# Performance work log

Hardware: AMD Instinct MI355X
Metric: run time of the kernel (lower is better)

The kernel has to match this reference:

```python
import jax, jax.numpy as jnp
import numpy as np

B, S, IN, OUT = 4, 4096, 4096, 4096

def setup_inputs() -> dict:
    key = jax.random.key(0)
    k1, k2, k3 = jax.random.split(key, 3)
    x = jax.random.normal(k1, (B, S, IN), dtype=jnp.float32)
    # packed ternary weight: (sign+1) in {0,1,2}, stored as small int
    packed_w = jax.random.randint(k2, (OUT, IN), 0, 3, dtype=jnp.int32)
    # alpha = mean(|W|) surrogate; act_scale = max|x|/127 surrogate
    alpha = jnp.float32(0.02)
    act_scale = jnp.float32(4.0 / 127.0)
    bias = jax.random.normal(k3, (OUT,), dtype=jnp.float32)
    return {"x": x, "packed_w": packed_w, "alpha": alpha, "act_scale": act_scale, "bias": bias}

def reference(x, packed_w, alpha, act_scale, bias):
    # Activation fake-quant (int8 symmetric): round(x/scale), clamp, dequant.
    # torch uses act_scale.item() -> scale is a constant w.r.t. autodiff.
    scale = jax.lax.stop_gradient(jnp.maximum(act_scale, 1e-5))
    x_int = jnp.clip(jnp.round(x / scale), -127.0, 127.0)
    x_dq = jnp.nan_to_num(x_int * scale, nan=0.0, posinf=10000.0, neginf=-10000.0)
    # Ternary weight dequant: (packed - 1) * alpha, values in {-a, 0, +a}
    w = (packed_w.astype(jnp.float32) - 1.0) * alpha  # [OUT, IN]
    # F.linear: x @ W^T + b
    return jnp.einsum('bsi,oi->bso', x_dq, w) + bias
```

## Files before the change

### kernel.cpp

```cpp
#include <hip/hip_runtime.h>
#include <hip/hip_bf16.h>

typedef int v4i __attribute__((ext_vector_type(4)));

#define M_DIM 16384
#define N_DIM 4096
#define K_DIM 4096
#define BM 256
#define BN 256
#define BKB 128
#define NT (K_DIM / BKB)

__global__ void quant_x_kernel(const float4* __restrict__ x, int* __restrict__ q,
                               const float* __restrict__ act_scale, int n4) {
  const float s = fmaxf(act_scale[0], 1e-5f);
  int i = blockIdx.x * blockDim.x + threadIdx.x;
  const int stride = gridDim.x * blockDim.x;
  for (; i < n4; i += stride) {
    float4 v = x[i];
    int b0 = (int)fminf(fmaxf(rintf(v.x / s), -127.f), 127.f);
    int b1 = (int)fminf(fmaxf(rintf(v.y / s), -127.f), 127.f);
    int b2 = (int)fminf(fmaxf(rintf(v.z / s), -127.f), 127.f);
    int b3 = (int)fminf(fmaxf(rintf(v.w / s), -127.f), 127.f);
    q[i] = (b0 & 0xff) | ((b1 & 0xff) << 8) | ((b2 & 0xff) << 16) | ((b3 & 0xff) << 24);
  }
}

__global__ void pack_w_kernel(const int4* __restrict__ w, int* __restrict__ q, int n4) {
  int i = blockIdx.x * blockDim.x + threadIdx.x;
  const int stride = gridDim.x * blockDim.x;
  for (; i < n4; i += stride) {
    int4 v = w[i];
    q[i] = ((v.x - 1) & 0xff) | (((v.y - 1) & 0xff) << 8) |
           (((v.z - 1) & 0xff) << 16) | (((v.w - 1) & 0xff) << 24);
  }
}

__global__ __launch_bounds__(512, 2) void bitlinear_gemm(
    const signed char* __restrict__ A,
    const signed char* __restrict__ B,
    const float* __restrict__ bias,
    const float* __restrict__ alpha_p,
    const float* __restrict__ act_scale_p,
    float* __restrict__ out) {
  __shared__ __align__(16) signed char As[2][BM * BKB];
  __shared__ __align__(16) signed char Bs[2][BN * BKB];

  const int t = threadIdx.x;
  const int lane = t & 63, wid = t >> 6;
  const int wm = wid >> 2, wn = wid & 3;
  const int l15 = lane & 15, l4 = lane >> 4;

  const int nwg = (M_DIM / BM) * (N_DIM / BN);
  const int wg = (blockIdx.x & 7) * (nwg >> 3) + (blockIdx.x >> 3);
  const int bm = wg / (N_DIM / BN);
  const int bn = wg % (N_DIM / BN);

  const signed char* aGl = A + ((size_t)(bm * BM + (t >> 3))) * K_DIM + (t & 7) * 16;
  const signed char* bGl = B + ((size_t)(bn * BN + (t >> 3))) * K_DIM + (t & 7) * 16;
  const int wrOff = (t >> 3) * 128 + (((t & 7) ^ ((t >> 3) & 7)) * 16);

  v4i sA[4], sB[4];

#define GL_A(u, P) sA[u] = *(const v4i*)((P) + (size_t)((u) * 64) * K_DIM)
#define GL_B(u, P) sB[u] = *(const v4i*)((P) + (size_t)((u) * 64) * K_DIM)
#define WR_A(BUF) { _Pragma("unroll") for (int u = 0; u < 4; ++u) \
    *(v4i*)&As[BUF][u * 8192 + wrOff] = sA[u]; }
#define WR_B(BUF) { _Pragma("unroll") for (int u = 0; u < 4; ++u) \
    *(v4i*)&Bs[BUF][u * 8192 + wrOff] = sB[u]; }

  const int l7 = l15 & 7;
  const int soK0 = ((0 + l4) ^ l7) * 16;
  const int soK1 = ((4 + l4) ^ l7) * 16;
  const int aRd = (wm * 128 + l15) * BKB;
  const int bRd = (wn * 64 + l15) * BKB;

  v4i acc[8][4] = {};
  v4i bF[4][2], aF[2][2];

#define LOAD_B(buf) \
  { _Pragma("unroll") for (int nc = 0; nc < 4; ++nc) { \
      bF[nc][0] = *(const v4i*)&Bs[buf][bRd + nc * 2048 + soK0]; \
      bF[nc][1] = *(const v4i*)&Bs[buf][bRd + nc * 2048 + soK1]; } }

#define LOAD_A(buf, q) \
  aF[0][0] = *(const v4i*)&As[buf][aRd + (2*(q)) * 2048 + soK0]; \
  aF[0][1] = *(const v4i*)&As[buf][aRd + (2*(q)) * 2048 + soK1]; \
  aF[1][0] = *(const v4i*)&As[buf][aRd + (2*(q)+1) * 2048 + soK0]; \
  aF[1][1] = *(const v4i*)&As[buf][aRd + (2*(q)+1) * 2048 + soK1];

#define MFMA_Q(q) \
  { _Pragma("unroll") for (int nc = 0; nc < 4; ++nc) { \
      acc[2*(q)][nc]   = __builtin_amdgcn_mfma_i32_16x16x64_i8(aF[0][0], bF[nc][0], acc[2*(q)][nc], 0, 0, 0); \
      acc[2*(q)][nc]   = __builtin_amdgcn_mfma_i32_16x16x64_i8(aF[0][1], bF[nc][1], acc[2*(q)][nc], 0, 0, 0); \
      acc[2*(q)+1][nc] = __builtin_amdgcn_mfma_i32_16x16x64_i8(aF[1][0], bF[nc][0], acc[2*(q)+1][nc], 0, 0, 0); \
      acc[2*(q)+1][nc] = __builtin_amdgcn_mfma_i32_16x16x64_i8(aF[1][1], bF[nc][1], acc[2*(q)+1][nc], 0, 0, 0); } }

#define BAR __builtin_amdgcn_s_barrier()

#define TILE_BODY(BUF, PA, PB) do { \
    LOAD_B(BUF); LOAD_A(BUF, 0); \
    GL_B(0, PB); GL_B(1, PB); \
    __builtin_amdgcn_s_setprio(1); MFMA_Q(0); __builtin_amdgcn_s_setprio(0); \
    LOAD_A(BUF, 1); \
    GL_B(2, PB); GL_B(3, PB); \
    __builtin_amdgcn_s_setprio(1); MFMA_Q(1); __builtin_amdgcn_s_setprio(0); \
    LOAD_A(BUF, 2); \
    GL_A(0, PA); GL_A(1, PA); GL_A(2, PA); GL_A(3, PA); \
    __builtin_amdgcn_s_setprio(1); MFMA_Q(2); __builtin_amdgcn_s_setprio(0); \
    WR_B(BUF^1); \
    LOAD_A(BUF, 3); \
    __builtin_amdgcn_s_setprio(1); MFMA_Q(3); __builtin_amdgcn_s_setprio(0); \
    WR_A(BUF^1); \
    asm volatile("s_waitcnt lgkmcnt(0)" ::: "memory"); \
    BAR; \
  } while (0)

  GL_B(0, bGl); GL_B(1, bGl); GL_B(2, bGl); GL_B(3, bGl);
  GL_A(0, aGl); GL_A(1, aGl); GL_A(2, aGl); GL_A(3, aGl);
  asm volatile("s_waitcnt vmcnt(0)" ::: "memory");
  WR_B(0); WR_A(0);
  asm volatile("s_waitcnt lgkmcnt(0)" ::: "memory");
  BAR;
  __builtin_amdgcn_sched_barrier(0);

  const signed char* aGk = aGl;
  const signed char* bGk = bGl;
  for (int it = 0; it < NT / 2 - 1; ++it) {
    TILE_BODY(0, aGk + BKB,     bGk + BKB);
    TILE_BODY(1, aGk + 2 * BKB, bGk + 2 * BKB);
    aGk += 2 * BKB; bGk += 2 * BKB;
  }
  TILE_BODY(0, aGk + BKB, bGk + BKB);
  TILE_BODY(1, aGk + BKB, bGk + BKB);

  const float sA_ = fmaxf(act_scale_p[0], 1e-5f) * alpha_p[0];
  const int gn0 = bn * BN + wn * 64 + l15;
  const int gm0 = bm * BM + wm * 128 + l4 * 4;
#pragma unroll
  for (int nc = 0; nc < 4; ++nc) {
    const float bv = bias[gn0 + nc * 16];
#pragma unroll
    for (int mr = 0; mr < 8; ++mr) {
#pragma unroll
      for (int r = 0; r < 4; ++r) {
        const int gm = gm0 + mr * 16 + r;
        out[(size_t)gm * N_DIM + gn0 + nc * 16] = (float)acc[mr][nc][r] * sA_ + bv;
      }
    }
  }
}

extern "C" void kernel_launch(void* const* d_in, const int* in_sizes, int n_in,
                              void* d_out, int out_size, void* d_ws, size_t ws_size,
                              hipStream_t stream) {
  const float* x      = (const float*)d_in[0];
  const int*   pw     = (const int*)d_in[1];
  const float* alpha  = (const float*)d_in[2];
  const float* act_sc = (const float*)d_in[3];
  const float* bias   = (const float*)d_in[4];
  float* out = (float*)d_out;

  signed char* x8 = (signed char*)d_ws;
  signed char* w8 = (signed char*)d_ws + (size_t)M_DIM * K_DIM;

  quant_x_kernel<<<2048, 256, 0, stream>>>((const float4*)x, (int*)x8, act_sc, M_DIM * K_DIM / 4);
  pack_w_kernel<<<2048, 256, 0, stream>>>((const int4*)pw, (int*)w8, N_DIM * K_DIM / 4);

  dim3 grid((M_DIM / BM) * (N_DIM / BN));
  bitlinear_gemm<<<grid, 512, 0, stream>>>(x8, w8, bias, alpha, act_sc, out);
}
```

Before: 380.1 us.

## Load A fragments directly from global memory into registers, bypassing LDS

The int8 activation tile no longer goes through shared memory. Each wave loads its MFMA A-operand fragments straight from global memory into two ping-ponged register sets, prefetching the next quarter during the current MFMA group. This removes the LDS writes and reads for A and halves the LDS footprint, which may allow higher occupancy. In exchange, A data that was shared through LDS is now re-read from global or L2 by each of the four waves in a row, and the fragment loads are uncoalesced 16-byte strided accesses whose latency must hide behind a single MFMA quarter.

```diff
diff --git a/kernel.cpp b/kernel.cpp
--- a/kernel.cpp
+++ b/kernel.cpp
@@ -43,7 +43,6 @@
     const float* __restrict__ alpha_p,
     const float* __restrict__ act_scale_p,
     float* __restrict__ out) {
-  __shared__ __align__(16) signed char As[2][BM * BKB];
   __shared__ __align__(16) signed char Bs[2][BN * BKB];
 
   const int t = threadIdx.x;
@@ -56,83 +55,78 @@
   const int bm = wg / (N_DIM / BN);
   const int bn = wg % (N_DIM / BN);
 
-  const signed char* aGl = A + ((size_t)(bm * BM + (t >> 3))) * K_DIM + (t & 7) * 16;
   const signed char* bGl = B + ((size_t)(bn * BN + (t >> 3))) * K_DIM + (t & 7) * 16;
   const int wrOff = (t >> 3) * 128 + (((t & 7) ^ ((t >> 3) & 7)) * 16);
+  v4i sB[4];
 
-  v4i sA[4], sB[4];
-
-#define GL_A(u, P) sA[u] = *(const v4i*)((P) + (size_t)((u) * 64) * K_DIM)
 #define GL_B(u, P) sB[u] = *(const v4i*)((P) + (size_t)((u) * 64) * K_DIM)
-#define WR_A(BUF) { _Pragma("unroll") for (int u = 0; u < 4; ++u) \
-    *(v4i*)&As[BUF][u * 8192 + wrOff] = sA[u]; }
 #define WR_B(BUF) { _Pragma("unroll") for (int u = 0; u < 4; ++u) \
     *(v4i*)&Bs[BUF][u * 8192 + wrOff] = sB[u]; }
 
   const int l7 = l15 & 7;
   const int soK0 = ((0 + l4) ^ l7) * 16;
   const int soK1 = ((4 + l4) ^ l7) * 16;
-  const int aRd = (wm * 128 + l15) * BKB;
   const int bRd = (wn * 64 + l15) * BKB;
 
+  const signed char* aBase = A + ((size_t)(bm * BM + wm * 128 + l15)) * K_DIM + l4 * 16;
+
+  v4i aP[4], aQ[4];
+#define AL(R, mi2, KOFF) \
+  R[0] = *(const v4i*)(aBase + (size_t)(mi2) * 16 * K_DIM + (KOFF)); \
+  R[1] = *(const v4i*)(aBase + (size_t)(mi2) * 16 * K_DIM + (KOFF) + 64); \
+  R[2] = *(const v4i*)(aBase + (size_t)((mi2) + 1) * 16 * K_DIM + (KOFF)); \
+  R[3] = *(const v4i*)(aBase + (size_t)((mi2) + 1) * 16 * K_DIM + (KOFF) + 64);
+
   v4i acc[8][4] = {};
-  v4i bF[4][2], aF[2][2];
+  v4i bF[4][2];
 
 #define LOAD_B(buf) \
   { _Pragma("unroll") for (int nc = 0; nc < 4; ++nc) { \
       bF[nc][0] = *(const v4i*)&Bs[buf][bRd + nc * 2048 + soK0]; \
       bF[nc][1] = *(const v4i*)&Bs[buf][bRd + nc * 2048 + soK1]; } }
 
-#define LOAD_A(buf, q) \
-  aF[0][0] = *(const v4i*)&As[buf][aRd + (2*(q)) * 2048 + soK0]; \
-  aF[0][1] = *(const v4i*)&As[buf][aRd + (2*(q)) * 2048 + soK1]; \
-  aF[1][0] = *(const v4i*)&As[buf][aRd + (2*(q)+1) * 2048 + soK0]; \
-  aF[1][1] = *(const v4i*)&As[buf][aRd + (2*(q)+1) * 2048 + soK1];
-
-#define MFMA_Q(q) \
+#define MFMA_Q(q, R) \
   { _Pragma("unroll") for (int nc = 0; nc < 4; ++nc) { \
-      acc[2*(q)][nc]   = __builtin_amdgcn_mfma_i32_16x16x64_i8(aF[0][0], bF[nc][0], acc[2*(q)][nc], 0, 0, 0); \
-      acc[2*(q)][nc]   = __builtin_amdgcn_mfma_i32_16x16x64_i8(aF[0][1], bF[nc][1], acc[2*(q)][nc], 0, 0, 0); \
-      acc[2*(q)+1][nc] = __builtin_amdgcn_mfma_i32_16x16x64_i8(aF[1][0], bF[nc][0], acc[2*(q)+1][nc], 0, 0, 0); \
-      acc[2*(q)+1][nc] = __builtin_amdgcn_mfma_i32_16x16x64_i8(aF[1][1], bF[nc][1], acc[2*(q)+1][nc], 0, 0, 0); } }
+      acc[2*(q)][nc]   = __builtin_amdgcn_mfma_i32_16x16x64_i8(R[0], bF[nc][0], acc[2*(q)][nc], 0, 0, 0); \
+      acc[2*(q)][nc]   = __builtin_amdgcn_mfma_i32_16x16x64_i8(R[1], bF[nc][1], acc[2*(q)][nc], 0, 0, 0); \
+      acc[2*(q)+1][nc] = __builtin_amdgcn_mfma_i32_16x16x64_i8(R[2], bF[nc][0], acc[2*(q)+1][nc], 0, 0, 0); \
+      acc[2*(q)+1][nc] = __builtin_amdgcn_mfma_i32_16x16x64_i8(R[3], bF[nc][1], acc[2*(q)+1][nc], 0, 0, 0); } }
 
 #define BAR __builtin_amdgcn_s_barrier()
 
-#define TILE_BODY(BUF, PA, PB) do { \
-    LOAD_B(BUF); LOAD_A(BUF, 0); \
+#define TILE_BODY(BUF, KCUR, KNEXT, PB) do { \
     GL_B(0, PB); GL_B(1, PB); \
-    __builtin_amdgcn_s_setprio(1); MFMA_Q(0); __builtin_amdgcn_s_setprio(0); \
-    LOAD_A(BUF, 1); \
+    LOAD_B(BUF); \
+    AL(aQ, 2, KCUR); \
+    __builtin_amdgcn_s_setprio(1); MFMA_Q(0, aP); __builtin_amdgcn_s_setprio(0); \
     GL_B(2, PB); GL_B(3, PB); \
-    __builtin_amdgcn_s_setprio(1); MFMA_Q(1); __builtin_amdgcn_s_setprio(0); \
-    LOAD_A(BUF, 2); \
-    GL_A(0, PA); GL_A(1, PA); GL_A(2, PA); GL_A(3, PA); \
-    __builtin_amdgcn_s_setprio(1); MFMA_Q(2); __builtin_amdgcn_s_setprio(0); \
+    AL(aP, 4, KCUR); \
+    __builtin_amdgcn_s_setprio(1); MFMA_Q(1, aQ); __builtin_amdgcn_s_setprio(0); \
+    AL(aQ, 6, KCUR); \
+    __builtin_amdgcn_s_setprio(1); MFMA_Q(2, aP); __builtin_amdgcn_s_setprio(0); \
     WR_B(BUF^1); \
-    LOAD_A(BUF, 3); \
-    __builtin_amdgcn_s_setprio(1); MFMA_Q(3); __builtin_amdgcn_s_setprio(0); \
-    WR_A(BUF^1); \
+    AL(aP, 0, KNEXT); \
+    __builtin_amdgcn_s_setprio(1); MFMA_Q(3, aQ); __builtin_amdgcn_s_setprio(0); \
     asm volatile("s_waitcnt lgkmcnt(0)" ::: "memory"); \
     BAR; \
   } while (0)
 
   GL_B(0, bGl); GL_B(1, bGl); GL_B(2, bGl); GL_B(3, bGl);
-  GL_A(0, aGl); GL_A(1, aGl); GL_A(2, aGl); GL_A(3, aGl);
-  asm volatile("s_waitcnt vmcnt(0)" ::: "memory");
-  WR_B(0); WR_A(0);
+  AL(aP, 0, 0);
+  WR_B(0);
   asm volatile("s_waitcnt lgkmcnt(0)" ::: "memory");
   BAR;
   __builtin_amdgcn_sched_barrier(0);
 
-  const signed char* aGk = aGl;
   const signed char* bGk = bGl;
+  int koff = 0;
   for (int it = 0; it < NT / 2 - 1; ++it) {
-    TILE_BODY(0, aGk + BKB,     bGk + BKB);
-    TILE_BODY(1, aGk + 2 * BKB, bGk + 2 * BKB);
-    aGk += 2 * BKB; bGk += 2 * BKB;
+    TILE_BODY(0, koff,       koff + BKB,     bGk + BKB);
+    TILE_BODY(1, koff + BKB, koff + 2 * BKB, bGk + 2 * BKB);
+    koff += 2 * BKB; bGk += 2 * BKB;
   }
-  TILE_BODY(0, aGk + BKB, bGk + BKB);
-  TILE_BODY(1, aGk + BKB, bGk + BKB);
+  TILE_BODY(0, koff, koff + BKB, bGk + BKB);
+  TILE_BODY(1, koff + BKB, koff + BKB, bGk + BKB);
 
   const float sA_ = fmaxf(act_scale_p[0], 1e-5f) * alpha_p[0];
   const int gn0 = bn * BN + wn * 64 + l15;
```

Result: slower. 669.3 us (+76.1%).

## Stream GEMM tiles straight into LDS with global_load_lds

Applied to the files above, without the earlier changes.

Global-to-shared staging of the int8 A and B tiles no longer goes through registers and ds_write; it now uses direct global_load_lds transfers of 16 bytes per lane into ping-pong LDS buffers. The XOR swizzle moves onto the global source address, so the LDS layout seen by the MFMA fragment reads stays the same. All DMA for the next tile is issued at the start of each tile body and waited on with vmcnt(0) before the barrier. This frees the staging VGPRs and removes the LDS write instructions, at the cost of issuing every copy up front rather than interleaving them with the MFMA quarters.

```diff
diff --git a/kernel.cpp b/kernel.cpp
--- a/kernel.cpp
+++ b/kernel.cpp
@@ -43,8 +43,10 @@
     const float* __restrict__ alpha_p,
     const float* __restrict__ act_scale_p,
     float* __restrict__ out) {
-  __shared__ __align__(16) signed char As[2][BM * BKB];
-  __shared__ __align__(16) signed char Bs[2][BN * BKB];
+  __shared__ __align__(16) signed char As0[BM * BKB];
+  __shared__ __align__(16) signed char As1[BM * BKB];
+  __shared__ __align__(16) signed char Bs0[BN * BKB];
+  __shared__ __align__(16) signed char Bs1[BN * BKB];
 
   const int t = threadIdx.x;
   const int lane = t & 63, wid = t >> 6;
@@ -56,18 +58,18 @@
   const int bm = wg / (N_DIM / BN);
   const int bn = wg % (N_DIM / BN);
 
-  const signed char* aGl = A + ((size_t)(bm * BM + (t >> 3))) * K_DIM + (t & 7) * 16;
-  const signed char* bGl = B + ((size_t)(bn * BN + (t >> 3))) * K_DIM + (t & 7) * 16;
-  const int wrOff = (t >> 3) * 128 + (((t & 7) ^ ((t >> 3) & 7)) * 16);
+  const int dmaSeg = wid * 4096;
+  const signed char* aD = A + ((size_t)(bm * BM + 32 * wid + (lane >> 3))) * K_DIM
+                            + (((lane & 7) ^ (lane >> 3)) * 16);
+  const signed char* bD = B + ((size_t)(bn * BN + 32 * wid + (lane >> 3))) * K_DIM
+                            + (((lane & 7) ^ (lane >> 3)) * 16);
 
-  v4i sA[4], sB[4];
-
-#define GL_A(u, P) sA[u] = *(const v4i*)((P) + (size_t)((u) * 64) * K_DIM)
-#define GL_B(u, P) sB[u] = *(const v4i*)((P) + (size_t)((u) * 64) * K_DIM)
-#define WR_A(BUF) { _Pragma("unroll") for (int u = 0; u < 4; ++u) \
-    *(v4i*)&As[BUF][u * 8192 + wrOff] = sA[u]; }
-#define WR_B(BUF) { _Pragma("unroll") for (int u = 0; u < 4; ++u) \
-    *(v4i*)&Bs[BUF][u * 8192 + wrOff] = sB[u]; }
+#define DMA4(SRCBASE, DSTARR, KOFF) \
+  { _Pragma("unroll") for (int i = 0; i < 4; ++i) \
+      __builtin_amdgcn_global_load_lds( \
+        (const __attribute__((address_space(1))) void*)((SRCBASE) + (size_t)(8 * i) * K_DIM + (KOFF)), \
+        (__attribute__((address_space(3))) void*)(&(DSTARR)[dmaSeg + i * 1024]), \
+        16, 0, 0); }
 
   const int l7 = l15 & 7;
   const int soK0 = ((0 + l4) ^ l7) * 16;
@@ -78,16 +80,16 @@
   v4i acc[8][4] = {};
   v4i bF[4][2], aF[2][2];
 
-#define LOAD_B(buf) \
+#define LOAD_B(BS) \
   { _Pragma("unroll") for (int nc = 0; nc < 4; ++nc) { \
-      bF[nc][0] = *(const v4i*)&Bs[buf][bRd + nc * 2048 + soK0]; \
-      bF[nc][1] = *(const v4i*)&Bs[buf][bRd + nc * 2048 + soK1]; } }
+      bF[nc][0] = *(const v4i*)&(BS)[bRd + nc * 2048 + soK0]; \
+      bF[nc][1] = *(const v4i*)&(BS)[bRd + nc * 2048 + soK1]; } }
 
-#define LOAD_A(buf, q) \
-  aF[0][0] = *(const v4i*)&As[buf][aRd + (2*(q)) * 2048 + soK0]; \
-  aF[0][1] = *(const v4i*)&As[buf][aRd + (2*(q)) * 2048 + soK1]; \
-  aF[1][0] = *(const v4i*)&As[buf][aRd + (2*(q)+1) * 2048 + soK0]; \
-  aF[1][1] = *(const v4i*)&As[buf][aRd + (2*(q)+1) * 2048 + soK1];
+#define LOAD_A(AS, q) \
+  aF[0][0] = *(const v4i*)&(AS)[aRd + (2*(q)) * 2048 + soK0]; \
+  aF[0][1] = *(const v4i*)&(AS)[aRd + (2*(q)) * 2048 + soK1]; \
+  aF[1][0] = *(const v4i*)&(AS)[aRd + (2*(q)+1) * 2048 + soK0]; \
+  aF[1][1] = *(const v4i*)&(AS)[aRd + (2*(q)+1) * 2048 + soK1];
 
 #define MFMA_Q(q) \
   { _Pragma("unroll") for (int nc = 0; nc < 4; ++nc) { \
@@ -98,41 +100,33 @@
 
 #define BAR __builtin_amdgcn_s_barrier()
 
-#define TILE_BODY(BUF, PA, PB) do { \
-    LOAD_B(BUF); LOAD_A(BUF, 0); \
-    GL_B(0, PB); GL_B(1, PB); \
+#define TILE_BODY(ASR, BSR, ASW, BSW, KNEXT) do { \
+    DMA4(bD, BSW, KNEXT); \
+    DMA4(aD, ASW, KNEXT); \
+    LOAD_B(BSR); LOAD_A(ASR, 0); \
     __builtin_amdgcn_s_setprio(1); MFMA_Q(0); __builtin_amdgcn_s_setprio(0); \
-    LOAD_A(BUF, 1); \
-    GL_B(2, PB); GL_B(3, PB); \
+    LOAD_A(ASR, 1); \
     __builtin_amdgcn_s_setprio(1); MFMA_Q(1); __builtin_amdgcn_s_setprio(0); \
-    LOAD_A(BUF, 2); \
-    GL_A(0, PA); GL_A(1, PA); GL_A(2, PA); GL_A(3, PA); \
+    LOAD_A(ASR, 2); \
     __builtin_amdgcn_s_setprio(1); MFMA_Q(2); __builtin_amdgcn_s_setprio(0); \
-    WR_B(BUF^1); \
-    LOAD_A(BUF, 3); \
+    LOAD_A(ASR, 3); \
     __builtin_amdgcn_s_setprio(1); MFMA_Q(3); __builtin_amdgcn_s_setprio(0); \
-    WR_A(BUF^1); \
-    asm volatile("s_waitcnt lgkmcnt(0)" ::: "memory"); \
+    asm volatile("s_waitcnt vmcnt(0) lgkmcnt(0)" ::: "memory"); \
     BAR; \
   } while (0)
 
-  GL_B(0, bGl); GL_B(1, bGl); GL_B(2, bGl); GL_B(3, bGl);
-  GL_A(0, aGl); GL_A(1, aGl); GL_A(2, aGl); GL_A(3, aGl);
+  DMA4(bD, Bs0, 0);
+  DMA4(aD, As0, 0);
   asm volatile("s_waitcnt vmcnt(0)" ::: "memory");
-  WR_B(0); WR_A(0);
-  asm volatile("s_waitcnt lgkmcnt(0)" ::: "memory");
   BAR;
   __builtin_amdgcn_sched_barrier(0);
 
-  const signed char* aGk = aGl;
-  const signed char* bGk = bGl;
   for (int it = 0; it < NT / 2 - 1; ++it) {
-    TILE_BODY(0, aGk + BKB,     bGk + BKB);
-    TILE_BODY(1, aGk + 2 * BKB, bGk + 2 * BKB);
-    aGk += 2 * BKB; bGk += 2 * BKB;
+    TILE_BODY(As0, Bs0, As1, Bs1, (2 * it + 1) * BKB);
+    TILE_BODY(As1, Bs1, As0, Bs0, (2 * it + 2) * BKB);
   }
-  TILE_BODY(0, aGk + BKB, bGk + BKB);
-  TILE_BODY(1, aGk + BKB, bGk + BKB);
+  TILE_BODY(As0, Bs0, As1, Bs1, 31 * BKB);
+  TILE_BODY(As1, Bs1, As0, Bs0, 31 * BKB);
 
   const float sA_ = fmaxf(act_scale_p[0], 1e-5f) * alpha_p[0];
   const int gn0 = bn * BN + wn * 64 + l15;
```

New measurement: 402.8 us. 6.0% more time.

## Switch int8 GEMM to 32x32x32 MFMA tiles and use reciprocal in quantization

Applied to the files above, without the earlier changes.

Replaces the 16x16x64 int8 MFMA instructions with 32x32x32 ones. Fragment loads, the swizzled LDS read offsets, accumulator layout and epilogue indexing are reorganized to fit the larger tile, with each wave covering 4x2 tiles of 32x32. The goal is to cut the number of LDS fragment reads and MFMA issues per unit of work, since each B fragment is reused across more rows. The activation quantization kernel also multiplies by a precomputed reciprocal instead of dividing, which can change rounding in rare ties.

```diff
diff --git a/kernel.cpp b/kernel.cpp
--- a/kernel.cpp
+++ b/kernel.cpp
@@ -1,7 +1,8 @@
 #include <hip/hip_runtime.h>
 #include <hip/hip_bf16.h>
 
-typedef int v4i __attribute__((ext_vector_type(4)));
+typedef int v4i  __attribute__((ext_vector_type(4)));
+typedef int v16i __attribute__((ext_vector_type(16)));
 
 #define M_DIM 16384
 #define N_DIM 4096
@@ -14,14 +15,15 @@
 __global__ void quant_x_kernel(const float4* __restrict__ x, int* __restrict__ q,
                                const float* __restrict__ act_scale, int n4) {
   const float s = fmaxf(act_scale[0], 1e-5f);
+  const float inv_s = 1.0f / s;
   int i = blockIdx.x * blockDim.x + threadIdx.x;
   const int stride = gridDim.x * blockDim.x;
   for (; i < n4; i += stride) {
     float4 v = x[i];
-    int b0 = (int)fminf(fmaxf(rintf(v.x / s), -127.f), 127.f);
-    int b1 = (int)fminf(fmaxf(rintf(v.y / s), -127.f), 127.f);
-    int b2 = (int)fminf(fmaxf(rintf(v.z / s), -127.f), 127.f);
-    int b3 = (int)fminf(fmaxf(rintf(v.w / s), -127.f), 127.f);
+    int b0 = (int)fminf(fmaxf(rintf(v.x * inv_s), -127.f), 127.f);
+    int b1 = (int)fminf(fmaxf(rintf(v.y * inv_s), -127.f), 127.f);
+    int b2 = (int)fminf(fmaxf(rintf(v.z * inv_s), -127.f), 127.f);
+    int b3 = (int)fminf(fmaxf(rintf(v.w * inv_s), -127.f), 127.f);
     q[i] = (b0 & 0xff) | ((b1 & 0xff) << 8) | ((b2 & 0xff) << 16) | ((b3 & 0xff) << 24);
   }
 }
@@ -49,7 +51,7 @@
   const int t = threadIdx.x;
   const int lane = t & 63, wid = t >> 6;
   const int wm = wid >> 2, wn = wid & 3;
-  const int l15 = lane & 15, l4 = lane >> 4;
+  const int l31 = lane & 31, l5 = lane >> 5;
 
   const int nwg = (M_DIM / BM) * (N_DIM / BN);
   const int wg = (blockIdx.x & 7) * (nwg >> 3) + (blockIdx.x >> 3);
@@ -69,48 +71,47 @@
 #define WR_B(BUF) { _Pragma("unroll") for (int u = 0; u < 4; ++u) \
     *(v4i*)&Bs[BUF][u * 8192 + wrOff] = sB[u]; }
 
-  const int l7 = l15 & 7;
-  const int soK0 = ((0 + l4) ^ l7) * 16;
-  const int soK1 = ((4 + l4) ^ l7) * 16;
-  const int aRd = (wm * 128 + l15) * BKB;
-  const int bRd = (wn * 64 + l15) * BKB;
+  const int x7 = l31 & 7;
+#define CS(ks) ((((ks) * 2 + l5) ^ x7) * 16)
+  const int aRd = (wm * 128 + l31) * BKB;
+  const int bRd = (wn * 64 + l31) * BKB;
 
-  v4i acc[8][4] = {};
-  v4i bF[4][2], aF[2][2];
+  v16i acc[4][2] = {};
+  v4i bF[2][4];
+  v4i aF[4];
 
-#define LOAD_B(buf) \
-  { _Pragma("unroll") for (int nc = 0; nc < 4; ++nc) { \
-      bF[nc][0] = *(const v4i*)&Bs[buf][bRd + nc * 2048 + soK0]; \
-      bF[nc][1] = *(const v4i*)&Bs[buf][bRd + nc * 2048 + soK1]; } }
+#define LOAD_B32(buf) \
+  { _Pragma("unroll") for (int nt = 0; nt < 2; ++nt) { \
+      _Pragma("unroll") for (int ks = 0; ks < 4; ++ks) { \
+        bF[nt][ks] = *(const v4i*)&Bs[buf][bRd + nt * 4096 + CS(ks)]; } } }
 
-#define LOAD_A(buf, q) \
-  aF[0][0] = *(const v4i*)&As[buf][aRd + (2*(q)) * 2048 + soK0]; \
-  aF[0][1] = *(const v4i*)&As[buf][aRd + (2*(q)) * 2048 + soK1]; \
-  aF[1][0] = *(const v4i*)&As[buf][aRd + (2*(q)+1) * 2048 + soK0]; \
-  aF[1][1] = *(const v4i*)&As[buf][aRd + (2*(q)+1) * 2048 + soK1];
+#define LOAD_A32(buf, mt) \
+  { _Pragma("unroll") for (int ks = 0; ks < 4; ++ks) { \
+      aF[ks] = *(const v4i*)&As[buf][aRd + (mt) * 4096 + CS(ks)]; } }
 
-#define MFMA_Q(q) \
-  { _Pragma("unroll") for (int nc = 0; nc < 4; ++nc) { \
-      acc[2*(q)][nc]   = __builtin_amdgcn_mfma_i32_16x16x64_i8(aF[0][0], bF[nc][0], acc[2*(q)][nc], 0, 0, 0); \
-      acc[2*(q)][nc]   = __builtin_amdgcn_mfma_i32_16x16x64_i8(aF[0][1], bF[nc][1], acc[2*(q)][nc], 0, 0, 0); \
-      acc[2*(q)+1][nc] = __builtin_amdgcn_mfma_i32_16x16x64_i8(aF[1][0], bF[nc][0], acc[2*(q)+1][nc], 0, 0, 0); \
-      acc[2*(q)+1][nc] = __builtin_amdgcn_mfma_i32_16x16x64_i8(aF[1][1], bF[nc][1], acc[2*(q)+1][nc], 0, 0, 0); } }
+#define MT(mt) \
+  { _Pragma("unroll") for (int ks = 0; ks < 4; ++ks) { \
+      acc[mt][0] = __builtin_amdgcn_mfma_i32_32x32x32_i8(aF[ks], bF[0][ks], acc[mt][0], 0, 0, 0); \
+      acc[mt][1] = __builtin_amdgcn_mfma_i32_32x32x32_i8(aF[ks], bF[1][ks], acc[mt][1], 0, 0, 0); } }
 
 #define BAR __builtin_amdgcn_s_barrier()
+#define PRIO1 __builtin_amdgcn_s_setprio(1)
+#define PRIO0 __builtin_amdgcn_s_setprio(0)
 
 #define TILE_BODY(BUF, PA, PB) do { \
-    LOAD_B(BUF); LOAD_A(BUF, 0); \
+    LOAD_B32(BUF); \
+    LOAD_A32(BUF, 0); \
     GL_B(0, PB); GL_B(1, PB); \
-    __builtin_amdgcn_s_setprio(1); MFMA_Q(0); __builtin_amdgcn_s_setprio(0); \
-    LOAD_A(BUF, 1); \
+    PRIO1; MT(0); PRIO0; \
+    LOAD_A32(BUF, 1); \
     GL_B(2, PB); GL_B(3, PB); \
-    __builtin_amdgcn_s_setprio(1); MFMA_Q(1); __builtin_amdgcn_s_setprio(0); \
-    LOAD_A(BUF, 2); \
+    PRIO1; MT(1); PRIO0; \
+    LOAD_A32(BUF, 2); \
     GL_A(0, PA); GL_A(1, PA); GL_A(2, PA); GL_A(3, PA); \
-    __builtin_amdgcn_s_setprio(1); MFMA_Q(2); __builtin_amdgcn_s_setprio(0); \
+    PRIO1; MT(2); PRIO0; \
     WR_B(BUF^1); \
-    LOAD_A(BUF, 3); \
-    __builtin_amdgcn_s_setprio(1); MFMA_Q(3); __builtin_amdgcn_s_setprio(0); \
+    LOAD_A32(BUF, 3); \
+    PRIO1; MT(3); PRIO0; \
     WR_A(BUF^1); \
     asm volatile("s_waitcnt lgkmcnt(0)" ::: "memory"); \
     BAR; \
@@ -135,17 +136,17 @@
   TILE_BODY(1, aGk + BKB, bGk + BKB);
 
   const float sA_ = fmaxf(act_scale_p[0], 1e-5f) * alpha_p[0];
-  const int gn0 = bn * BN + wn * 64 + l15;
-  const int gm0 = bm * BM + wm * 128 + l4 * 4;
+  const int gn0 = bn * BN + wn * 64 + l31;
+  const int gm0 = bm * BM + wm * 128 + 4 * l5;
 #pragma unroll
-  for (int nc = 0; nc < 4; ++nc) {
-    const float bv = bias[gn0 + nc * 16];
+  for (int nt = 0; nt < 2; ++nt) {
+    const float bv = bias[gn0 + nt * 32];
 #pragma unroll
-    for (int mr = 0; mr < 8; ++mr) {
+    for (int mt = 0; mt < 4; ++mt) {
 #pragma unroll
-      for (int r = 0; r < 4; ++r) {
-        const int gm = gm0 + mr * 16 + r;
-        out[(size_t)gm * N_DIM + gn0 + nc * 16] = (float)acc[mr][nc][r] * sA_ + bv;
+      for (int r = 0; r < 16; ++r) {
+        const int gm = gm0 + mt * 32 + (r & 3) + 8 * (r >> 2);
+        out[(size_t)gm * N_DIM + gn0 + nt * 32] = (float)acc[mt][nt][r] * sA_ + bv;
       }
     }
   }
```

Result: no change. 385.2 us (+1.4%).
